# Kernel tuning notes

Measured on AMD Instinct MI355X. Metric: run time of the kernel, lower is better.

## Reference

```python
import jax, jax.numpy as jnp
import numpy as np


def setup_inputs() -> dict:
    key = jax.random.key(0)
    k1, k2, k3 = jax.random.split(key, 3)
    B, C, Q, D = 64, 512, 64, 512
    H = jax.random.normal(k1, (B, C, D), dtype=jnp.float32)
    U = jax.random.normal(k2, (B, Q, D), dtype=jnp.float32)
    w = jax.random.normal(k3, (3 * D, 1), dtype=jnp.float32) * 0.02
    return {"H": H, "U": U, "w": w}


def reference(H, U, w):
    # Original: S[b,c,q] = concat([H[b,c], U[b,q], H[b,c]*U[b,q]]) @ w
    # Algebraically: split w = [w_h; w_u; w_hu] (each [D]) ->
    #   S = (H @ w_h)[:, :, None] + (U @ w_u)[:, None, :] + (H * w_hu) @ U^T
    D = H.shape[-1]
    w = w[:, 0]
    w_h, w_u, w_hu = w[:D], w[D:2 * D], w[2 * D:]
    s_h = jnp.einsum('bcd,d->bc', H, w_h)          # [B, C]
    s_u = jnp.einsum('bqd,d->bq', U, w_u)          # [B, Q]
    s_hu = jnp.einsum('bcd,bqd->bcq', H * w_hu, U)  # [B, C, Q]
    return s_h[:, :, None] + s_u[:, None, :] + s_hu
```

## Files before the change

kernel.cpp:

```cpp
#include <hip/hip_runtime.h>
#include <hip/hip_bf16.h>


#define Bn 64
#define Cn 512
#define Qn 64
#define Dn 512

typedef __bf16 bf16x8 __attribute__((ext_vector_type(8)));
typedef float  f32x4  __attribute__((ext_vector_type(4)));

__global__ __launch_bounds__(512, 1)
void sim_kernel(const float* __restrict__ H, const float* __restrict__ U,
                const float* __restrict__ w, float* __restrict__ out)
{
    __shared__ __bf16 Us[16][4][64][8];
    __shared__ float  su_l[Qn];

    const int r  = (int)blockIdx.x;
    const int x  = r & 7;
    const int i  = r >> 3;
    const int b  = x * 8 + (i >> 2);
    const int c0 = (i & 3) * 128;

    const int t    = (int)threadIdx.x;
    const int wv   = t >> 6;
    const int lane = t & 63;
    const int ql   = lane & 15;
    const int hh   = lane >> 4;

    const float* __restrict__ hp =
        H + ((size_t)(b * Cn + c0 + wv * 16 + ql)) * Dn + hh * 8;
    f32x4 ha[4], hb[4];
#pragma unroll
    for (int p = 0; p < 3; ++p) {
        ha[p] = *(const f32x4*)(hp + 32 * p);
        hb[p] = *(const f32x4*)(hp + 32 * p + 4);
    }

    {
        const int dk = t & 31;
        const int qg = t >> 5;
        const int kt = dk >> 1;
        const int cs = kt & 7;
        float su_p[4] = {0.f, 0.f, 0.f, 0.f};
#pragma unroll
        for (int half = 0; half < 2; ++half) {
            const int d0 = dk * 16 + half * 8;
            const int hv = (dk & 1) * 2 + half;
            f32x4 wh0 = *(const f32x4*)(w + d0);
            f32x4 wh1 = *(const f32x4*)(w + d0 + 4);
            f32x4 wu0 = *(const f32x4*)(w + 512 + d0);
            f32x4 wu1 = *(const f32x4*)(w + 512 + d0 + 4);
            f32x4 wm0 = *(const f32x4*)(w + 1024 + d0);
            f32x4 wm1 = *(const f32x4*)(w + 1024 + d0 + 4);
#pragma unroll
            for (int qi = 0; qi < 4; ++qi) {
                const int q = qg * 4 + qi;
                const float* __restrict__ Uq =
                    U + ((size_t)(b * Qn + q)) * Dn + d0;
                f32x4 u0 = *(const f32x4*)Uq;
                f32x4 u1 = *(const f32x4*)(Uq + 4);
                bf16x8 v;
#pragma unroll
                for (int e = 0; e < 4; ++e) {
                    su_p[qi] += wu0[e] * u0[e] + wu1[e] * u1[e];
                    v[e]     = (__bf16)__builtin_fmaf(wm0[e], u0[e], wh0[e]);
                    v[e + 4] = (__bf16)__builtin_fmaf(wm1[e], u1[e], wh1[e]);
                }
                *(bf16x8*)&Us[kt][hv][q ^ cs][0] = v;
            }
        }
#pragma unroll
        for (int qi = 0; qi < 4; ++qi) {
            float v = su_p[qi];
            v += __shfl_xor(v, 1);
            v += __shfl_xor(v, 2);
            v += __shfl_xor(v, 4);
            v += __shfl_xor(v, 8);
            v += __shfl_xor(v, 16);
            if (dk == 0) su_l[qg * 4 + qi] = v;
        }
    }

    __syncthreads();

    f32x4 acc[4] = {{0.f,0.f,0.f,0.f},{0.f,0.f,0.f,0.f},
                    {0.f,0.f,0.f,0.f},{0.f,0.f,0.f,0.f}};

#pragma unroll
    for (int k = 0; k < 16; ++k) {
        f32x4 ca = ha[k & 3], cb = hb[k & 3];
        if (k + 3 < 16) {
            ha[(k + 3) & 3] = *(const f32x4*)(hp + 32 * (k + 3));
            hb[(k + 3) & 3] = *(const f32x4*)(hp + 32 * (k + 3) + 4);
        }
        bf16x8 a;
#pragma unroll
        for (int e = 0; e < 4; ++e) {
            a[e]     = (__bf16)ca[e];
            a[e + 4] = (__bf16)cb[e];
        }
        const int pq = ql ^ (k & 7);
        bf16x8 f0 = *(const bf16x8*)&Us[k][hh][pq +  0][0];
        bf16x8 f1 = *(const bf16x8*)&Us[k][hh][pq + 16][0];
        bf16x8 f2 = *(const bf16x8*)&Us[k][hh][pq + 32][0];
        bf16x8 f3 = *(const bf16x8*)&Us[k][hh][pq + 48][0];
        acc[0] = __builtin_amdgcn_mfma_f32_16x16x32_bf16(a, f0, acc[0], 0, 0, 0);
        acc[1] = __builtin_amdgcn_mfma_f32_16x16x32_bf16(a, f1, acc[1], 0, 0, 0);
        acc[2] = __builtin_amdgcn_mfma_f32_16x16x32_bf16(a, f2, acc[2], 0, 0, 0);
        acc[3] = __builtin_amdgcn_mfma_f32_16x16x32_bf16(a, f3, acc[3], 0, 0, 0);
    }

    float* __restrict__ outb = out + ((size_t)(b * Cn + c0 + wv * 16)) * Qn;
#pragma unroll
    for (int n = 0; n < 4; ++n) {
        const int q = n * 16 + ql;
        const float s = su_l[q];
#pragma unroll
        for (int rr = 0; rr < 4; ++rr)
            outb[(size_t)(hh * 4 + rr) * Qn + q] = acc[n][rr] + s;
    }
}

extern "C" void kernel_launch(void* const* d_in, const int* in_sizes, int n_in,
                              void* d_out, int out_size, void* d_ws, size_t ws_size,
                              hipStream_t stream) {
    const float* H = (const float*)d_in[0];
    const float* U = (const float*)d_in[1];
    const float* w = (const float*)d_in[2];
    float* out = (float*)d_out;
    sim_kernel<<<dim3(256), dim3(512), 0, stream>>>(H, U, w, out);
}
```

Baseline: 20.91 us.

## Split U staging into two phases and overlap with early MFMA steps

The U-fused staging is remapped so each lane handles one q row and each wave a d-slice, with loop-uniform indices hoisted via readfirstlane. Only the first quarter of K is staged before the first barrier; the remaining slots are staged before the first four MFMA steps, with a second barrier before the rest. The shuffle-based su reduction is replaced by per-wave partial sums in shared memory, summed at output time. This aims to overlap staging with compute and cut the cross-lane reduction, at the cost of an extra barrier and extra LDS reads in the epilogue.

```diff
diff --git a/kernel.cpp b/kernel.cpp
--- a/kernel.cpp
+++ b/kernel.cpp
@@ -15,7 +15,7 @@
                 const float* __restrict__ w, float* __restrict__ out)
 {
     __shared__ __bf16 Us[16][4][64][8];
-    __shared__ float  su_l[Qn];
+    __shared__ float  su_p[8][64];
 
     const int r  = (int)blockIdx.x;
     const int x  = r & 7;
@@ -38,58 +38,36 @@
         hb[p] = *(const f32x4*)(hp + 32 * p + 4);
     }
 
-    {
-        const int dk = t & 31;
-        const int qg = t >> 5;
-        const int kt = dk >> 1;
-        const int cs = kt & 7;
-        float su_p[4] = {0.f, 0.f, 0.f, 0.f};
+    const float* __restrict__ Ubase = U + ((size_t)(b * Qn + lane)) * Dn;
+    float su_acc = 0.f;
+
+    auto stage_slot = [&](int j) {
+        const int slot = t + 512 * j;
+        const int kt = __builtin_amdgcn_readfirstlane(slot >> 8);
+        const int hv = __builtin_amdgcn_readfirstlane((slot >> 6) & 3);
+        const int d0 = kt * 32 + hv * 8;
+        f32x4 u0  = *(const f32x4*)(Ubase + d0);
+        f32x4 u1  = *(const f32x4*)(Ubase + d0 + 4);
+        f32x4 wh0 = *(const f32x4*)(w + d0);
+        f32x4 wh1 = *(const f32x4*)(w + d0 + 4);
+        f32x4 wu0 = *(const f32x4*)(w + 512 + d0);
+        f32x4 wu1 = *(const f32x4*)(w + 512 + d0 + 4);
+        f32x4 wm0 = *(const f32x4*)(w + 1024 + d0);
+        f32x4 wm1 = *(const f32x4*)(w + 1024 + d0 + 4);
+        bf16x8 v;
 #pragma unroll
-        for (int half = 0; half < 2; ++half) {
-            const int d0 = dk * 16 + half * 8;
-            const int hv = (dk & 1) * 2 + half;
-            f32x4 wh0 = *(const f32x4*)(w + d0);
-            f32x4 wh1 = *(const f32x4*)(w + d0 + 4);
-            f32x4 wu0 = *(const f32x4*)(w + 512 + d0);
-            f32x4 wu1 = *(const f32x4*)(w + 512 + d0 + 4);
-            f32x4 wm0 = *(const f32x4*)(w + 1024 + d0);
-            f32x4 wm1 = *(const f32x4*)(w + 1024 + d0 + 4);
-#pragma unroll
-            for (int qi = 0; qi < 4; ++qi) {
-                const int q = qg * 4 + qi;
-                const float* __restrict__ Uq =
-                    U + ((size_t)(b * Qn + q)) * Dn + d0;
-                f32x4 u0 = *(const f32x4*)Uq;
-                f32x4 u1 = *(const f32x4*)(Uq + 4);
-                bf16x8 v;
-#pragma unroll
-                for (int e = 0; e < 4; ++e) {
-                    su_p[qi] += wu0[e] * u0[e] + wu1[e] * u1[e];
-                    v[e]     = (__bf16)__builtin_fmaf(wm0[e], u0[e], wh0[e]);
-                    v[e + 4] = (__bf16)__builtin_fmaf(wm1[e], u1[e], wh1[e]);
-                }
-                *(bf16x8*)&Us[kt][hv][q ^ cs][0] = v;
-            }
+        for (int e = 0; e < 4; ++e) {
+            su_acc += wu0[e] * u0[e] + wu1[e] * u1[e];
+            v[e]     = (__bf16)__builtin_fmaf(wm0[e], u0[e], wh0[e]);
+            v[e + 4] = (__bf16)__builtin_fmaf(wm1[e], u1[e], wh1[e]);
         }
-#pragma unroll
-        for (int qi = 0; qi < 4; ++qi) {
-            float v = su_p[qi];
-            v += __shfl_xor(v, 1);
-            v += __shfl_xor(v, 2);
-            v += __shfl_xor(v, 4);
-            v += __shfl_xor(v, 8);
-            v += __shfl_xor(v, 16);
-            if (dk == 0) su_l[qg * 4 + qi] = v;
-        }
-    }
-
-    __syncthreads();
+        *(bf16x8*)&Us[kt][hv][lane ^ (kt & 7)][0] = v;
+    };
 
     f32x4 acc[4] = {{0.f,0.f,0.f,0.f},{0.f,0.f,0.f,0.f},
                     {0.f,0.f,0.f,0.f},{0.f,0.f,0.f,0.f}};
 
-#pragma unroll
-    for (int k = 0; k < 16; ++k) {
+    auto compute_step = [&](int k) {
         f32x4 ca = ha[k & 3], cb = hb[k & 3];
         if (k + 3 < 16) {
             ha[(k + 3) & 3] = *(const f32x4*)(hp + 32 * (k + 3));
@@ -110,13 +88,29 @@
         acc[1] = __builtin_amdgcn_mfma_f32_16x16x32_bf16(a, f1, acc[1], 0, 0, 0);
         acc[2] = __builtin_amdgcn_mfma_f32_16x16x32_bf16(a, f2, acc[2], 0, 0, 0);
         acc[3] = __builtin_amdgcn_mfma_f32_16x16x32_bf16(a, f3, acc[3], 0, 0, 0);
-    }
+    };
+
+    stage_slot(0);
+    stage_slot(1);
+    __syncthreads();
+
+    stage_slot(2); stage_slot(3); stage_slot(4);
+    stage_slot(5); stage_slot(6); stage_slot(7);
+    su_p[wv][lane] = su_acc;
+
+    compute_step(0); compute_step(1); compute_step(2); compute_step(3);
+    __syncthreads();
+
+#pragma unroll
+    for (int k = 4; k < 16; ++k) compute_step(k);
 
     float* __restrict__ outb = out + ((size_t)(b * Cn + c0 + wv * 16)) * Qn;
 #pragma unroll
     for (int n = 0; n < 4; ++n) {
         const int q = n * 16 + ql;
-        const float s = su_l[q];
+        float s = 0.f;
+#pragma unroll
+        for (int pw = 0; pw < 8; ++pw) s += su_p[pw][q];
 #pragma unroll
         for (int rr = 0; rr < 4; ++rr)
             outb[(size_t)(hh * 4 + rr) * Qn + q] = acc[n][rr] + s;
```

After: 20.06 us (median of 2 runs). 4.1% less time.
